# Optimization experiments

Measured on AMD Instinct MI355X. Metric: run time of the kernel, lower is better.

Reference implementation:

```python
import jax, jax.numpy as jnp
import numpy as np

B, C, NH = 2, 128, 4
H = W = D = 28
WS = 7
SHIFT = 3
N = WS * WS * WS            # 343 tokens per window
HD = C // NH                # 32
SCALE = HD ** -0.5
HIDDEN = int(C * 4.0)
EPS = 1e-5


def _rel_pos_index():
    coords = np.stack(np.meshgrid(np.arange(WS), np.arange(WS), np.arange(WS), indexing='ij'))
    cf = coords.reshape(3, -1)                      # (3, N)
    rel = cf[:, :, None] - cf[:, None, :]           # (3, N, N)
    rel = rel.transpose(1, 2, 0) + (WS - 1)         # (N, N, 3), shifted to >=0
    idx = rel[..., 0] * (2 * WS - 1) ** 2 + rel[..., 1] * (2 * WS - 1) + rel[..., 2]
    return jnp.asarray(idx, dtype=jnp.int32)        # (N, N)


def setup_inputs() -> dict:
    key = jax.random.key(0)
    ks = jax.random.split(key, 16)
    s = 0.02
    return {
        'x': jax.random.normal(ks[0], (B, H * W * D, C), jnp.float32),
        'norm1_w': jnp.ones((C,), jnp.float32),
        'norm1_b': jnp.zeros((C,), jnp.float32),
        'qkv_w': jax.random.normal(ks[1], (3 * C, C), jnp.float32) * s,
        'qkv_b': jnp.zeros((3 * C,), jnp.float32),
        'rpb_table': jax.random.normal(ks[2], ((2 * WS - 1) ** 3, NH), jnp.float32) * s,
        'proj_w': jax.random.normal(ks[3], (C, C), jnp.float32) * s,
        'proj_b': jnp.zeros((C,), jnp.float32),
        'norm2_w': jnp.ones((C,), jnp.float32),
        'norm2_b': jnp.zeros((C,), jnp.float32),
        'mlp_w1': jax.random.normal(ks[4], (HIDDEN, C), jnp.float32) * s,
        'mlp_b1': jnp.zeros((HIDDEN,), jnp.float32),
        'mlp_w2': jax.random.normal(ks[5], (C, HIDDEN), jnp.float32) * s,
        'mlp_b2': jnp.zeros((C,), jnp.float32),
        'rel_idx': _rel_pos_index(),
    }


def _layernorm(x, w, b):
    mu = jnp.mean(x, axis=-1, keepdims=True)
    var = jnp.mean(jnp.square(x - mu), axis=-1, keepdims=True)
    return (x - mu) * jax.lax.rsqrt(var + EPS) * w + b


def _window_partition(x):
    # (B,H,W,D,C) -> (B*nW, N, C)
    x = x.reshape(B, H // WS, WS, W // WS, WS, D // WS, WS, C)
    x = x.transpose(0, 1, 3, 5, 2, 4, 6, 7)
    return x.reshape(-1, N, C)


def _window_reverse(wins):
    # (B*nW, N, C) -> (B,H,W,D,C)
    x = wins.reshape(B, H // WS, W // WS, D // WS, WS, WS, WS, C)
    x = x.transpose(0, 1, 4, 2, 5, 3, 6, 7)
    return x.reshape(B, H, W, D, C)


def _window_attention(xw, qkv_w, qkv_b, rpb_table, rel_idx, proj_w, proj_b):
    Bw = xw.shape[0]
    qkv = xw @ qkv_w.T + qkv_b                       # (Bw, N, 3C)
    qkv = qkv.reshape(Bw, N, 3, NH, HD).transpose(2, 0, 3, 1, 4)
    q, k, v = qkv[0], qkv[1], qkv[2]                 # each (Bw, NH, N, HD)
    attn = jnp.einsum('bhnd,bhmd->bhnm', q * SCALE, k)
    bias = rpb_table[rel_idx.reshape(-1)].reshape(N, N, NH).transpose(2, 0, 1)
    attn = jax.nn.softmax(attn + bias[None], axis=-1)
    out = jnp.einsum('bhnm,bhmd->bhnd', attn, v)     # (Bw, NH, N, HD)
    out = out.transpose(0, 2, 1, 3).reshape(Bw, N, C)
    return out @ proj_w.T + proj_b


def reference(x, norm1_w, norm1_b, qkv_w, qkv_b, rpb_table, proj_w, proj_b,
              norm2_w, norm2_b, mlp_w1, mlp_b1, mlp_w2, mlp_b2, rel_idx):
    shortcut = x
    h = _layernorm(x, norm1_w, norm1_b).reshape(B, H, W, D, C)
    if SHIFT > 0:
        h = jnp.roll(h, shift=(-SHIFT, -SHIFT, -SHIFT), axis=(1, 2, 3))
    wins = _window_partition(h)
    wins = _window_attention(wins, qkv_w, qkv_b, rpb_table, rel_idx, proj_w, proj_b)
    h = _window_reverse(wins)
    if SHIFT > 0:
        h = jnp.roll(h, shift=(SHIFT, SHIFT, SHIFT), axis=(1, 2, 3))
    x = shortcut + h.reshape(B, H * W * D, C)
    m = _layernorm(x, norm2_w, norm2_b)
    m = jax.nn.gelu(m @ mlp_w1.T + mlp_b1, approximate=False) @ mlp_w2.T + mlp_b2
    return x + m
```

## Files before the change

### kernel.cpp

```cpp
#include <hip/hip_runtime.h>

typedef __bf16 bfv8 __attribute__((ext_vector_type(8)));
typedef float f32x4 __attribute__((ext_vector_type(4)));
#define MFMA16(a,b,c) __builtin_amdgcn_mfma_f32_16x16x32_bf16(a,b,c,0,0,0)

constexpr int C      = 128;
constexpr int HD     = 32;
constexpr int NTOK   = 343;
constexpr int ROWS   = 43904;
constexpr int HIDDEN = 512;
constexpr float SCALE = 0.17677669529663687f;
constexpr float EPS   = 1e-5f;
constexpr int NT = 22;

static __device__ __forceinline__ float b2f(ushort u) {
  union { unsigned int i; float f; } x; x.i = ((unsigned int)u) << 16; return x.f;
}
static __device__ __forceinline__ ushort f2b(float f) {
  union { float f; unsigned int i; } x; x.f = f;
  unsigned int r = x.i + 0x7fffu + ((x.i >> 16) & 1u);
  return (ushort)(r >> 16);
}

static __device__ __forceinline__ int perm_row(int row) {
  int win = row / NTOK, tok = row - win * NTOK;
  int bb = win >> 6, wi = win & 63;
  int a  = wi >> 4, w2 = (wi >> 2) & 3, c2 = wi & 3;
  int t1 = tok / 49, rem = tok - t1 * 49;
  int t2 = rem / 7,  t3 = rem - t2 * 7;
  int gh = a * 7 + t1 + 3;  if (gh >= 28) gh -= 28;
  int gw = w2 * 7 + t2 + 3; if (gw >= 28) gw -= 28;
  int gd = c2 * 7 + t3 + 3; if (gd >= 28) gd -= 28;
  return bb * 21952 + gh * 784 + gw * 28 + gd;
}

__global__ __launch_bounds__(256) void cvt_kernel(const float* __restrict__ s0,
                                                  const float* __restrict__ s1,
                                                  const float* __restrict__ s2,
                                                  const float* __restrict__ s3,
                                                  ushort* __restrict__ d0,
                                                  ushort* __restrict__ d1,
                                                  ushort* __restrict__ d2,
                                                  ushort* __restrict__ d3) {
  int t = blockIdx.x * 256 + threadIdx.x;
  if (t < 49152)       d0[t]          = f2b(s0[t]);
  else if (t < 65536)  d1[t - 49152]  = f2b(s1[t - 49152]);
  else if (t < 131072) d2[t - 65536]  = f2b(s2[t - 65536]);
  else                 d3[t - 131072] = f2b(s3[t - 131072]);
}

__global__ __launch_bounds__(256) void bias_kernel(const int* __restrict__ rel,
                                                   const float* __restrict__ tab,
                                                   float4* __restrict__ biasr) {
  int t = blockIdx.x * 256 + threadIdx.x;
  if (t >= 4 * NT * NT * 64) return;
  int lane = t & 63;
  int nt   = (t >> 6) % NT;
  int mt   = ((t >> 6) / NT) % NT;
  int head = t / (64 * NT * NT);
  int k  = nt * 16 + (lane & 15);
  int qb = mt * 16 + (lane >> 4) * 4;
  float vv[4];
  #pragma unroll
  for (int r = 0; r < 4; ++r) {
    int q = qb + r;
    if (q < NTOK && k < NTOK) {
      int idx = rel[q * NTOK + k];
      vv[r] = tab[idx * 4 + head];
    } else {
      vv[r] = -3e38f;
    }
  }
  biasr[t] = make_float4(vv[0], vv[1], vv[2], vv[3]);
}

template<bool PERM>
__global__ __launch_bounds__(256) void ln_kernel(const float* __restrict__ in,
                                                 const float* __restrict__ w,
                                                 const float* __restrict__ b,
                                                 ushort* __restrict__ out) {
  int wid = threadIdx.x >> 6, lane = threadIdx.x & 63;
  int row = blockIdx.x * 4 + wid;
  int src = PERM ? perm_row(row) : row;
  float2 v = *reinterpret_cast<const float2*>(in + (size_t)src * C + lane * 2);
  float s = v.x + v.y, q = v.x * v.x + v.y * v.y;
  #pragma unroll
  for (int off = 32; off; off >>= 1) { s += __shfl_xor(s, off); q += __shfl_xor(q, off); }
  float mu = s * (1.0f / 128.0f);
  float var = q * (1.0f / 128.0f) - mu * mu;
  float rs = rsqrtf(var + EPS);
  int c = lane * 2;
  ushort2 ov;
  ov.x = f2b((v.x - mu) * rs * w[c]     + b[c]);
  ov.y = f2b((v.y - mu) * rs * w[c + 1] + b[c + 1]);
  *reinterpret_cast<ushort2*>(out + (size_t)row * C + c) = ov;
}

template<int KTOT, int EPI>
__global__ __launch_bounds__(256) void gemm_kernel(const ushort* __restrict__ A,
                                                   const ushort* __restrict__ W,
                                                   const float* __restrict__ bias,
                                                   const float* __restrict__ X,
                                                   ushort* __restrict__ O0,
                                                   ushort* __restrict__ O1,
                                                   ushort* __restrict__ O2,
                                                   float* __restrict__ OF) {
  __shared__ ushort Al[128][136];
  __shared__ ushort Bl[128][136];
  const int m0 = blockIdx.x * 128, n0 = blockIdx.y * 128;
  const int tid = threadIdx.x, lane = tid & 63, wid = tid >> 6;
  const int wr = wid >> 1, wc = wid & 1;
  const int lr = lane & 15, kb0 = (lane >> 4) * 8;
  const int sr = tid >> 4, sc = (tid & 15) * 8;
  f32x4 acc[4][4] = {};
  for (int kc = 0; kc < KTOT; kc += 128) {
    #pragma unroll
    for (int p = 0; p < 8; ++p) {
      int row = p * 16 + sr;
      *reinterpret_cast<int4*>(&Al[row][sc]) =
          *reinterpret_cast<const int4*>(&A[(size_t)(m0 + row) * KTOT + kc + sc]);
      *reinterpret_cast<int4*>(&Bl[row][sc]) =
          *reinterpret_cast<const int4*>(&W[(size_t)(n0 + row) * KTOT + kc + sc]);
    }
    __syncthreads();
    #pragma unroll
    for (int kk = 0; kk < 4; ++kk) {
      int kb = kk * 32 + kb0;
      bfv8 a[4], b[4];
      #pragma unroll
      for (int m = 0; m < 4; ++m) a[m] = *reinterpret_cast<const bfv8*>(&Al[wr * 64 + m * 16 + lr][kb]);
      #pragma unroll
      for (int n = 0; n < 4; ++n) b[n] = *reinterpret_cast<const bfv8*>(&Bl[wc * 64 + n * 16 + lr][kb]);
      #pragma unroll
      for (int m = 0; m < 4; ++m)
        #pragma unroll
        for (int n = 0; n < 4; ++n)
          acc[m][n] = MFMA16(a[m], b[n], acc[m][n]);
    }
    __syncthreads();
  }
  #pragma unroll
  for (int m = 0; m < 4; ++m)
    #pragma unroll
    for (int n = 0; n < 4; ++n)
      #pragma unroll
      for (int r = 0; r < 4; ++r) {
        int gm = m0 + wr * 64 + m * 16 + (lane >> 4) * 4 + r;
        int gn = n0 + wc * 64 + n * 16 + (lane & 15);
        float v = acc[m][n][r] + bias[gn];
        if (EPI == 0) {
          int which = gn >> 7, head = (gn >> 5) & 3, d = gn & 31;
          if (which == 0) v *= SCALE;
          int win = gm / NTOK, tok = gm - win * NTOK;
          ushort* dst = (which == 0) ? O0 : (which == 1) ? O1 : O2;
          dst[((win * 4 + head) * NTOK + tok) * HD + d] = f2b(v);
        } else {
          int orig = perm_row(gm);
          OF[(size_t)orig * C + gn] = v + X[(size_t)orig * C + gn];
        }
      }
}

__global__ __launch_bounds__(256) void mlp_kernel(const float* __restrict__ y,
                                                  const float* __restrict__ nw,
                                                  const float* __restrict__ nb,
                                                  const ushort* __restrict__ W1,
                                                  const float* __restrict__ b1,
                                                  const ushort* __restrict__ W2,
                                                  const float* __restrict__ b2,
                                                  float* __restrict__ outp) {
  __shared__ ushort Al[64][136];
  __shared__ ushort Hl[4][16][136];
  __shared__ ushort Wl[128][136];
  const int m0 = blockIdx.x * 64;
  const int tid = threadIdx.x, lane = tid & 63, wave = tid >> 6;
  {
    int sub = tid & 7;
    #pragma unroll
    for (int p = 0; p < 2; ++p) {
      int row = p * 32 + (tid >> 3);
      const float* yr = y + (size_t)(m0 + row) * C + sub * 16;
      float4 v0 = *reinterpret_cast<const float4*>(yr);
      float4 v1 = *reinterpret_cast<const float4*>(yr + 4);
      float4 v2 = *reinterpret_cast<const float4*>(yr + 8);
      float4 v3 = *reinterpret_cast<const float4*>(yr + 12);
      float s = v0.x + v0.y + v0.z + v0.w + v1.x + v1.y + v1.z + v1.w
              + v2.x + v2.y + v2.z + v2.w + v3.x + v3.y + v3.z + v3.w;
      float q = v0.x*v0.x + v0.y*v0.y + v0.z*v0.z + v0.w*v0.w
              + v1.x*v1.x + v1.y*v1.y + v1.z*v1.z + v1.w*v1.w
              + v2.x*v2.x + v2.y*v2.y + v2.z*v2.z + v2.w*v2.w
              + v3.x*v3.x + v3.y*v3.y + v3.z*v3.z + v3.w*v3.w;
      #pragma unroll
      for (int off = 1; off < 8; off <<= 1) { s += __shfl_xor(s, off); q += __shfl_xor(q, off); }
      float mu = s * (1.0f / 128.0f);
      float var = q * (1.0f / 128.0f) - mu * mu;
      float rs = rsqrtf(var + EPS);
      int c0 = sub * 16;
      float4 vv[4] = {v0, v1, v2, v3};
      #pragma unroll
      for (int j = 0; j < 4; ++j) {
        int c = c0 + j * 4;
        ushort4 o;
        o.x = f2b((vv[j].x - mu) * rs * nw[c]     + nb[c]);
        o.y = f2b((vv[j].y - mu) * rs * nw[c + 1] + nb[c + 1]);
        o.z = f2b((vv[j].z - mu) * rs * nw[c + 2] + nb[c + 2]);
        o.w = f2b((vv[j].w - mu) * rs * nw[c + 3] + nb[c + 3]);
        *reinterpret_cast<ushort4*>(&Al[row][c]) = o;
      }
    }
  }
  __syncthreads();
  const int lr = lane & 15, kb0 = (lane >> 4) * 8;
  const int key = lane & 15, qr4 = (lane >> 4) * 4;
  const int sr = tid >> 4, sc = (tid & 15) * 8;
  bfv8 af[4];
  #pragma unroll
  for (int kk = 0; kk < 4; ++kk)
    af[kk] = *reinterpret_cast<const bfv8*>(&Al[wave * 16 + lr][kk * 32 + kb0]);
  f32x4 acc[8] = {};
  for (int c = 0; c < 4; ++c) {
    #pragma unroll
    for (int p = 0; p < 8; ++p) {
      int row = p * 16 + sr;
      *reinterpret_cast<int4*>(&Wl[row][sc]) =
          *reinterpret_cast<const int4*>(&W1[(size_t)(c * 128 + row) * 128 + sc]);
    }
    __syncthreads();
    f32x4 hacc[8] = {};
    #pragma unroll
    for (int kk = 0; kk < 4; ++kk) {
      bfv8 a = af[kk];
      #pragma unroll
      for (int n = 0; n < 8; ++n) {
        bfv8 w = *reinterpret_cast<const bfv8*>(&Wl[n * 16 + lr][kk * 32 + kb0]);
        hacc[n] = MFMA16(a, w, hacc[n]);
      }
    }
    #pragma unroll
    for (int n = 0; n < 8; ++n)
      #pragma unroll
      for (int r = 0; r < 4; ++r) {
        float val = hacc[n][r] + b1[c * 128 + n * 16 + key];
        float g = 0.5f * val * (1.0f + erff(val * 0.70710678118654752f));
        Hl[wave][qr4 + r][n * 16 + key] = f2b(g);
      }
    bfv8 hf[4];
    #pragma unroll
    for (int kk = 0; kk < 4; ++kk)
      hf[kk] = *reinterpret_cast<const bfv8*>(&Hl[wave][lr][kk * 32 + kb0]);
    __syncthreads();
    #pragma unroll
    for (int p = 0; p < 8; ++p) {
      int row = p * 16 + sr;
      *reinterpret_cast<int4*>(&Wl[row][sc]) =
          *reinterpret_cast<const int4*>(&W2[(size_t)row * HIDDEN + c * 128 + sc]);
    }
    __syncthreads();
    #pragma unroll
    for (int kk = 0; kk < 4; ++kk) {
      bfv8 h = hf[kk];
      #pragma unroll
      for (int n = 0; n < 8; ++n) {
        bfv8 w = *reinterpret_cast<const bfv8*>(&Wl[n * 16 + lr][kk * 32 + kb0]);
        acc[n] = MFMA16(h, w, acc[n]);
      }
    }
    __syncthreads();
  }
  #pragma unroll
  for (int n = 0; n < 8; ++n)
    #pragma unroll
    for (int r = 0; r < 4; ++r) {
      int gm = m0 + wave * 16 + qr4 + r;
      int gn = n * 16 + key;
      outp[(size_t)gm * C + gn] = acc[n][r] + b2[gn] + y[(size_t)gm * C + gn];
    }
}

__global__ __launch_bounds__(512) void attn_kernel(const ushort* __restrict__ Q,
                                                   const ushort* __restrict__ K,
                                                   const ushort* __restrict__ V,
                                                   const f32x4* __restrict__ biasr,
                                                   ushort* __restrict__ out) {
  __shared__ ushort vt[32][360];
  __shared__ ushort pl[8][16][204];
  const int wh = blockIdx.x;
  const int win = wh >> 2, head = wh & 3;
  const int tid = threadIdx.x, lane = tid & 63, wave = tid >> 6;
  if (tid < 352) {
    int t = tid;
    if (t < NTOK) {
      ushort tmp[32];
      const ushort* vr = V + ((size_t)wh * NTOK + t) * HD;
      *reinterpret_cast<int4*>(&tmp[0])  = *reinterpret_cast<const int4*>(vr);
      *reinterpret_cast<int4*>(&tmp[8])  = *reinterpret_cast<const int4*>(vr + 8);
      *reinterpret_cast<int4*>(&tmp[16]) = *reinterpret_cast<const int4*>(vr + 16);
      *reinterpret_cast<int4*>(&tmp[24]) = *reinterpret_cast<const int4*>(vr + 24);
      #pragma unroll
      for (int d = 0; d < 32; ++d) vt[d][t] = tmp[d];
    } else {
      #pragma unroll
      for (int d = 0; d < 32; ++d) vt[d][t] = 0;
    }
  }
  __syncthreads();
  const int lr = lane & 15, kb0 = (lane >> 4) * 8;
  const int key = lane & 15, qr4 = (lane >> 4) * 4;
  for (int mt = wave; mt < NT; mt += 8) {
    int qrow = mt * 16 + lr; if (qrow > 342) qrow = 342;
    bfv8 aq = *reinterpret_cast<const bfv8*>(Q + ((size_t)wh * NTOK + qrow) * HD + kb0);
    const f32x4* bR = biasr + ((size_t)(head * NT + mt) * NT) * 64 + lane;
    float sm[4] = {0.f, 0.f, 0.f, 0.f};
    f32x4 o0 = {}, o1 = {};
    #pragma unroll
    for (int nt = 0; nt < 12; ++nt) {
      int krow = nt * 16 + lr;
      bfv8 bk = *reinterpret_cast<const bfv8*>(K + ((size_t)wh * NTOK + krow) * HD + kb0);
      f32x4 s = MFMA16(aq, bk, bR[nt * 64]);
      int kcol = nt * 16 + key;
      #pragma unroll
      for (int r = 0; r < 4; ++r) {
        float p = __expf(s[r]);
        sm[r] += p;
        pl[wave][qr4 + r][kcol] = f2b(p);
      }
    }
    #pragma unroll
    for (int kt = 0; kt < 6; ++kt) {
      bfv8 bp  = *reinterpret_cast<const bfv8*>(&pl[wave][lr][kt * 32 + kb0]);
      bfv8 av0 = *reinterpret_cast<const bfv8*>(&vt[lr][kt * 32 + kb0]);
      bfv8 av1 = *reinterpret_cast<const bfv8*>(&vt[16 + lr][kt * 32 + kb0]);
      o0 = MFMA16(av0, bp, o0);
      o1 = MFMA16(av1, bp, o1);
    }
    #pragma unroll
    for (int nt = 12; nt < NT; ++nt) {
      int krow = nt * 16 + lr; if (krow > 342) krow = 342;
      bfv8 bk = *reinterpret_cast<const bfv8*>(K + ((size_t)wh * NTOK + krow) * HD + kb0);
      f32x4 s = MFMA16(aq, bk, bR[nt * 64]);
      int kcol = (nt - 12) * 16 + key;
      #pragma unroll
      for (int r = 0; r < 4; ++r) {
        float p = __expf(s[r]);
        sm[r] += p;
        pl[wave][qr4 + r][kcol] = f2b(p);
      }
    }
    #pragma unroll
    for (int kt = 0; kt < 5; ++kt) {
      bfv8 bp  = *reinterpret_cast<const bfv8*>(&pl[wave][lr][kt * 32 + kb0]);
      bfv8 av0 = *reinterpret_cast<const bfv8*>(&vt[lr][192 + kt * 32 + kb0]);
      bfv8 av1 = *reinterpret_cast<const bfv8*>(&vt[16 + lr][192 + kt * 32 + kb0]);
      o0 = MFMA16(av0, bp, o0);
      o1 = MFMA16(av1, bp, o1);
    }
    #pragma unroll
    for (int r = 0; r < 4; ++r) {
      #pragma unroll
      for (int off = 1; off < 16; off <<= 1) sm[r] += __shfl_xor(sm[r], off);
    }
    float inv[4];
    #pragma unroll
    for (int r = 0; r < 4; ++r) inv[r] = 1.0f / sm[r];
    int qcol = lane & 15;
    int srcl = (qcol >> 2) << 4;
    float i0 = __shfl(inv[0], srcl), i1 = __shfl(inv[1], srcl);
    float i2 = __shfl(inv[2], srcl), i3 = __shfl(inv[3], srcl);
    float invq = (qcol & 2) ? ((qcol & 1) ? i3 : i2) : ((qcol & 1) ? i1 : i0);
    int q = mt * 16 + qcol;
    if (q < NTOK) {
      int dbase = qr4;
      ushort4 r0, r1;
      r0.x = f2b(o0[0] * invq); r0.y = f2b(o0[1] * invq);
      r0.z = f2b(o0[2] * invq); r0.w = f2b(o0[3] * invq);
      r1.x = f2b(o1[0] * invq); r1.y = f2b(o1[1] * invq);
      r1.z = f2b(o1[2] * invq); r1.w = f2b(o1[3] * invq);
      ushort* ob = out + (size_t)(win * NTOK + q) * C + head * HD;
      *reinterpret_cast<ushort4*>(ob + dbase)      = r0;
      *reinterpret_cast<ushort4*>(ob + 16 + dbase) = r1;
    }
  }
}

extern "C" void kernel_launch(void* const* d_in, const int* in_sizes, int n_in,
                              void* d_out, int out_size, void* d_ws, size_t ws_size,
                              hipStream_t stream) {
  const float* x     = (const float*)d_in[0];
  const float* n1w   = (const float*)d_in[1];
  const float* n1b   = (const float*)d_in[2];
  const float* qkvw  = (const float*)d_in[3];
  const float* qkvb  = (const float*)d_in[4];
  const float* rpb   = (const float*)d_in[5];
  const float* projw = (const float*)d_in[6];
  const float* projb = (const float*)d_in[7];
  const float* n2w   = (const float*)d_in[8];
  const float* n2b   = (const float*)d_in[9];
  const float* w1    = (const float*)d_in[10];
  const float* b1    = (const float*)d_in[11];
  const float* w2    = (const float*)d_in[12];
  const float* b2    = (const float*)d_in[13];
  const int*   rel   = (const int*)d_in[14];

  char* ws = (char*)d_ws;
  constexpr size_t SZ_ACT  = (size_t)ROWS * C * 2;
  constexpr size_t SZ_BIAS = (size_t)4 * NT * NT * 64 * 16;

  ushort* lnbuf  = (ushort*)(ws);
  ushort* Qb     = (ushort*)(ws + SZ_ACT);
  ushort* Kb     = (ushort*)(ws + 2 * SZ_ACT);
  ushort* Vb     = (ushort*)(ws + 3 * SZ_ACT);
  f32x4*  biasr  = (f32x4*)(ws + 4 * SZ_ACT);
  size_t off_att = (4 * SZ_ACT + SZ_BIAS + 255) & ~(size_t)255;
  ushort* attout = (ushort*)(ws + off_att);
  size_t off_y   = off_att + SZ_ACT;
  float*  y      = (float*)(ws + off_y);
  size_t off_w   = off_y + (size_t)ROWS * C * 4;
  ushort* wqkv   = (ushort*)(ws + off_w);
  ushort* wproj  = (ushort*)(ws + off_w + 98304);
  ushort* wm1    = (ushort*)(ws + off_w + 131072);
  ushort* wm2    = (ushort*)(ws + off_w + 262144);
  float*  outp   = (float*)d_out;

  cvt_kernel<<<768, 256, 0, stream>>>(qkvw, projw, w1, w2, wqkv, wproj, wm1, wm2);
  bias_kernel<<<(4 * NT * NT * 64 + 255) / 256, 256, 0, stream>>>(rel, rpb, (float4*)biasr);
  ln_kernel<true><<<ROWS / 4, 256, 0, stream>>>(x, n1w, n1b, lnbuf);
  gemm_kernel<128, 0><<<dim3(343, 3), 256, 0, stream>>>(lnbuf, wqkv, qkvb, nullptr, Qb, Kb, Vb, nullptr);
  attn_kernel<<<512, 512, 0, stream>>>(Qb, Kb, Vb, biasr, attout);
  gemm_kernel<128, 1><<<dim3(343, 1), 256, 0, stream>>>(attout, wproj, projb, x, nullptr, nullptr, nullptr, y);
  mlp_kernel<<<ROWS / 64, 256, 0, stream>>>(y, n2w, n2b, wm1, b1, wm2, b2, outp);
}
```

Measured before the change: 137.6 us.

## Double MLP row tile to 128 with 512 threads and share A/H LDS buffer

The fused MLP kernel now processes 128 rows per block with 8 waves instead of 64 rows with 4 waves. Each W1/W2 chunk loaded into LDS is therefore reused by twice as many rows, halving weight traffic per row. The LayerNorm output buffer is reused in place for the GELU hidden activations, and the LDS row stride is padded to 140. The GELU epilogue now runs per output column tile, which reduces live accumulators. The risks are fewer blocks (343) on the device and a larger block that may lower occupancy.

```diff
diff --git a/kernel.cpp b/kernel.cpp
--- a/kernel.cpp
+++ b/kernel.cpp
@@ -161,7 +161,7 @@
       }
 }
 
-__global__ __launch_bounds__(256) void mlp_kernel(const float* __restrict__ y,
+__global__ __launch_bounds__(512) void mlp_kernel(const float* __restrict__ y,
                                                   const float* __restrict__ nw,
                                                   const float* __restrict__ nb,
                                                   const ushort* __restrict__ W1,
@@ -169,103 +169,84 @@
                                                   const ushort* __restrict__ W2,
                                                   const float* __restrict__ b2,
                                                   float* __restrict__ outp) {
-  __shared__ ushort Al[64][136];
-  __shared__ ushort Hl[4][16][136];
-  __shared__ ushort Wl[128][136];
-  const int m0 = blockIdx.x * 64;
+  __shared__ ushort AH[128][140];
+  __shared__ ushort Wl[128][140];
+  const int m0 = blockIdx.x * 128;
   const int tid = threadIdx.x, lane = tid & 63, wave = tid >> 6;
   {
-    int sub = tid & 7;
-    #pragma unroll
-    for (int p = 0; p < 2; ++p) {
-      int row = p * 32 + (tid >> 3);
-      const float* yr = y + (size_t)(m0 + row) * C + sub * 16;
-      float4 v0 = *reinterpret_cast<const float4*>(yr);
-      float4 v1 = *reinterpret_cast<const float4*>(yr + 4);
-      float4 v2 = *reinterpret_cast<const float4*>(yr + 8);
-      float4 v3 = *reinterpret_cast<const float4*>(yr + 12);
-      float s = v0.x + v0.y + v0.z + v0.w + v1.x + v1.y + v1.z + v1.w
-              + v2.x + v2.y + v2.z + v2.w + v3.x + v3.y + v3.z + v3.w;
-      float q = v0.x*v0.x + v0.y*v0.y + v0.z*v0.z + v0.w*v0.w
-              + v1.x*v1.x + v1.y*v1.y + v1.z*v1.z + v1.w*v1.w
-              + v2.x*v2.x + v2.y*v2.y + v2.z*v2.z + v2.w*v2.w
-              + v3.x*v3.x + v3.y*v3.y + v3.z*v3.z + v3.w*v3.w;
-      #pragma unroll
-      for (int off = 1; off < 8; off <<= 1) { s += __shfl_xor(s, off); q += __shfl_xor(q, off); }
-      float mu = s * (1.0f / 128.0f);
-      float var = q * (1.0f / 128.0f) - mu * mu;
-      float rs = rsqrtf(var + EPS);
-      int c0 = sub * 16;
-      float4 vv[4] = {v0, v1, v2, v3};
-      #pragma unroll
-      for (int j = 0; j < 4; ++j) {
-        int c = c0 + j * 4;
-        ushort4 o;
-        o.x = f2b((vv[j].x - mu) * rs * nw[c]     + nb[c]);
-        o.y = f2b((vv[j].y - mu) * rs * nw[c + 1] + nb[c + 1]);
-        o.z = f2b((vv[j].z - mu) * rs * nw[c + 2] + nb[c + 2]);
-        o.w = f2b((vv[j].w - mu) * rs * nw[c + 3] + nb[c + 3]);
-        *reinterpret_cast<ushort4*>(&Al[row][c]) = o;
-      }
-    }
-  }
-  __syncthreads();
+    int row = tid >> 2, sub = tid & 3;
+    const float* yr = y + (size_t)(m0 + row) * C + sub * 32;
+    float4 v[8];
+    float s = 0.f, q = 0.f;
+    #pragma unroll
+    for (int j = 0; j < 8; ++j) {
+      v[j] = *reinterpret_cast<const float4*>(yr + j * 4);
+      s += v[j].x + v[j].y + v[j].z + v[j].w;
+      q += v[j].x * v[j].x + v[j].y * v[j].y + v[j].z * v[j].z + v[j].w * v[j].w;
+    }
+    s += __shfl_xor(s, 1); q += __shfl_xor(q, 1);
+    s += __shfl_xor(s, 2); q += __shfl_xor(q, 2);
+    float mu = s * (1.0f / 128.0f);
+    float var = q * (1.0f / 128.0f) - mu * mu;
+    float rs = rsqrtf(var + EPS);
+    #pragma unroll
+    for (int j = 0; j < 8; ++j) {
+      int c = sub * 32 + j * 4;
+      ushort4 o;
+      o.x = f2b((v[j].x - mu) * rs * nw[c]     + nb[c]);
+      o.y = f2b((v[j].y - mu) * rs * nw[c + 1] + nb[c + 1]);
+      o.z = f2b((v[j].z - mu) * rs * nw[c + 2] + nb[c + 2]);
+      o.w = f2b((v[j].w - mu) * rs * nw[c + 3] + nb[c + 3]);
+      *reinterpret_cast<ushort4*>(&AH[row][c]) = o;
+    }
+  }
   const int lr = lane & 15, kb0 = (lane >> 4) * 8;
   const int key = lane & 15, qr4 = (lane >> 4) * 4;
   const int sr = tid >> 4, sc = (tid & 15) * 8;
   bfv8 af[4];
   #pragma unroll
   for (int kk = 0; kk < 4; ++kk)
-    af[kk] = *reinterpret_cast<const bfv8*>(&Al[wave * 16 + lr][kk * 32 + kb0]);
+    af[kk] = *reinterpret_cast<const bfv8*>(&AH[wave * 16 + lr][kk * 32 + kb0]);
   f32x4 acc[8] = {};
   for (int c = 0; c < 4; ++c) {
-    #pragma unroll
-    for (int p = 0; p < 8; ++p) {
-      int row = p * 16 + sr;
+    __syncthreads();
+    #pragma unroll
+    for (int p = 0; p < 4; ++p) {
+      int row = p * 32 + sr;
       *reinterpret_cast<int4*>(&Wl[row][sc]) =
           *reinterpret_cast<const int4*>(&W1[(size_t)(c * 128 + row) * 128 + sc]);
     }
     __syncthreads();
-    f32x4 hacc[8] = {};
-    #pragma unroll
-    for (int kk = 0; kk < 4; ++kk) {
-      bfv8 a = af[kk];
-      #pragma unroll
-      for (int n = 0; n < 8; ++n) {
-        bfv8 w = *reinterpret_cast<const bfv8*>(&Wl[n * 16 + lr][kk * 32 + kb0]);
-        hacc[n] = MFMA16(a, w, hacc[n]);
+    #pragma unroll
+    for (int n = 0; n < 8; ++n) {
+      f32x4 h = {};
+      #pragma unroll
+      for (int kk = 0; kk < 4; ++kk)
+        h = MFMA16(af[kk], *reinterpret_cast<const bfv8*>(&Wl[n * 16 + lr][kk * 32 + kb0]), h);
+      #pragma unroll
+      for (int r = 0; r < 4; ++r) {
+        float val = h[r] + b1[c * 128 + n * 16 + key];
+        float g = 0.5f * val * (1.0f + erff(val * 0.70710678118654752f));
+        AH[wave * 16 + qr4 + r][n * 16 + key] = f2b(g);
       }
     }
-    #pragma unroll
-    for (int n = 0; n < 8; ++n)
-      #pragma unroll
-      for (int r = 0; r < 4; ++r) {
-        float val = hacc[n][r] + b1[c * 128 + n * 16 + key];
-        float g = 0.5f * val * (1.0f + erff(val * 0.70710678118654752f));
-        Hl[wave][qr4 + r][n * 16 + key] = f2b(g);
-      }
     bfv8 hf[4];
     #pragma unroll
     for (int kk = 0; kk < 4; ++kk)
-      hf[kk] = *reinterpret_cast<const bfv8*>(&Hl[wave][lr][kk * 32 + kb0]);
-    __syncthreads();
-    #pragma unroll
-    for (int p = 0; p < 8; ++p) {
-      int row = p * 16 + sr;
+      hf[kk] = *reinterpret_cast<const bfv8*>(&AH[wave * 16 + lr][kk * 32 + kb0]);
+    __syncthreads();
+    #pragma unroll
+    for (int p = 0; p < 4; ++p) {
+      int row = p * 32 + sr;
       *reinterpret_cast<int4*>(&Wl[row][sc]) =
           *reinterpret_cast<const int4*>(&W2[(size_t)row * HIDDEN + c * 128 + sc]);
     }
     __syncthreads();
     #pragma unroll
-    for (int kk = 0; kk < 4; ++kk) {
-      bfv8 h = hf[kk];
-      #pragma unroll
-      for (int n = 0; n < 8; ++n) {
-        bfv8 w = *reinterpret_cast<const bfv8*>(&Wl[n * 16 + lr][kk * 32 + kb0]);
-        acc[n] = MFMA16(h, w, acc[n]);
-      }
-    }
-    __syncthreads();
+    for (int n = 0; n < 8; ++n)
+      #pragma unroll
+      for (int kk = 0; kk < 4; ++kk)
+        acc[n] = MFMA16(hf[kk], *reinterpret_cast<const bfv8*>(&Wl[n * 16 + lr][kk * 32 + kb0]), acc[n]);
   }
   #pragma unroll
   for (int n = 0; n < 8; ++n)
@@ -427,5 +408,5 @@
   gemm_kernel<128, 0><<<dim3(343, 3), 256, 0, stream>>>(lnbuf, wqkv, qkvb, nullptr, Qb, Kb, Vb, nullptr);
   attn_kernel<<<512, 512, 0, stream>>>(Qb, Kb, Vb, biasr, attout);
   gemm_kernel<128, 1><<<dim3(343, 1), 256, 0, stream>>>(attout, wproj, projb, x, nullptr, nullptr, nullptr, y);
-  mlp_kernel<<<ROWS / 64, 256, 0, stream>>>(y, n2w, n2b, wm1, b1, wm2, b2, outp);
-}
+  mlp_kernel<<<ROWS / 128, 512, 0, stream>>>(y, n2w, n2b, wm1, b1, wm2, b2, outp);
+}
```

Measured after the change: 128.0 us. 7.0% less time.
